# Optimization experiments

Hardware: AMD Instinct MI355X
Metric: run time of the kernel (lower is better)

Reference implementation:

```python
import jax, jax.numpy as jnp
import numpy as np

# Model dims (Mamba2-2.7B-like)
B_SZ = 1; SEQ = 2048; HID = 2048
INTER = 4096; N_STATE = 128; N_GROUPS = 1; NH = 64; HD = 64
K_CONV = 4; CHUNK = 256
GN = N_GROUPS * N_STATE            # 128
CONV_DIM = INTER + 2 * GN          # 4352
D_IN = 2 * INTER + 2 * GN + NH     # 8512
EPS = 1e-5


def setup_inputs() -> dict:
    key = jax.random.key(0)
    ks = jax.random.split(key, 8)
    return {
        "hidden_states": jax.random.normal(ks[0], (B_SZ, SEQ, HID), jnp.float32),
        "W_in": jax.random.normal(ks[1], (HID, D_IN), jnp.float32) * 0.02,
        "conv_w": jax.random.normal(ks[2], (CONV_DIM, K_CONV), jnp.float32) * 0.2,
        "conv_b": jax.random.normal(ks[3], (CONV_DIM,), jnp.float32) * 0.1,
        "dt_bias": jax.random.uniform(ks[4], (NH,), jnp.float32, -4.0, 0.0),
        "A": -jnp.exp(jax.random.uniform(ks[5], (NH,), jnp.float32, -1.0, 1.0)),
        "D": jnp.ones((NH,), jnp.float32),
        "norm_weight": jnp.ones((INTER,), jnp.float32),
        "W_out": jax.random.normal(ks[6], (INTER, HID), jnp.float32) * 0.02,
    }


def reference(hidden_states, W_in, conv_w, conv_b, dt_bias, A, D, norm_weight, W_out):
    b, S, _ = hidden_states.shape
    # in_proj and split: gate [inter], x/B/C [conv_dim], dt [num_heads]
    proj = hidden_states @ W_in
    gate, xBC, dt = jnp.split(proj, [INTER, INTER + CONV_DIM], axis=-1)
    dt = jax.nn.softplus(dt + dt_bias)  # [b,S,NH]

    # causal depthwise conv1d + SiLU (kernel K, left-padded)
    xp = jnp.pad(xBC, ((0, 0), (K_CONV - 1, 0), (0, 0)))
    conv = conv_b
    for k in range(K_CONV):  # tiny fixed loop over kernel taps
        conv = conv + conv_w[:, k] * xp[:, k:k + S, :]
    xBC = jax.nn.silu(conv)

    x, Bm, Cm = jnp.split(xBC, [INTER, INTER + GN], axis=-1)
    L = CHUNK; nc = S // L
    x_c = x.reshape(b, nc, L, NH, HD)
    rep = NH // N_GROUPS
    B_c = jnp.repeat(Bm.reshape(b, nc, L, N_GROUPS, N_STATE), rep, axis=3)  # bclhn
    C_c = jnp.repeat(Cm.reshape(b, nc, L, N_GROUPS, N_STATE), rep, axis=3)
    dt_c = dt.reshape(b, nc, L, NH)

    dA = dt_c * A                      # [b,c,l,h]  (A < 0)
    cA = jnp.cumsum(dA, axis=2)        # within-chunk cumulative log-decay
    cAt = jnp.transpose(cA, (0, 1, 3, 2))  # [b,c,h,l]

    # intra-chunk: causal decay matrix, (C B^T) masked, weighted by dt
    diff = cAt[..., :, None] - cAt[..., None, :]          # [b,c,h,l,s]
    tril = jnp.tril(jnp.ones((L, L), bool))
    Lmat = jnp.exp(jnp.where(tril, diff, -jnp.inf))
    CB = jnp.einsum('bclhn,bcshn->bchls', C_c, B_c)
    M = CB * Lmat * jnp.transpose(dt_c, (0, 1, 3, 2))[:, :, :, None, :]
    Y_intra = jnp.einsum('bchls,bcshp->bclhp', M, x_c)

    # per-chunk end state contributions
    decay_states = jnp.exp(cA[:, :, -1:, :] - cA)          # [b,c,l,h]
    states = jnp.einsum('bclh,bclhn,bclhp->bchpn', decay_states * dt_c, B_c, x_c)
    chunk_decay = jnp.exp(cA[:, :, -1, :])                 # [b,c,h]

    def step(carry, inp):
        d, st = inp
        new = carry * d[..., None, None] + st
        return new, carry  # emit state entering the chunk

    _, prev = jax.lax.scan(step, jnp.zeros((b, NH, HD, N_STATE), states.dtype),
                           (jnp.moveaxis(chunk_decay, 1, 0), jnp.moveaxis(states, 1, 0)))
    prev = jnp.moveaxis(prev, 0, 1)                        # [b,c,h,p,n]

    Y_inter = jnp.einsum('bclhn,bclh,bchpn->bclhp', C_c, jnp.exp(cA), prev)
    Y = Y_intra + Y_inter + x_c * D[:, None]               # skip D*x per head

    y = Y.reshape(b, S, INTER)
    # gated RMSNorm in fp32
    z = y.astype(jnp.float32) * jax.nn.silu(gate.astype(jnp.float32))
    var = jnp.mean(z * z, axis=-1, keepdims=True)
    z = z * jax.lax.rsqrt(var + EPS) * norm_weight
    return z @ W_out
```

## Files before the change

kernel.cpp:

```cpp
#include <hip/hip_runtime.h>

typedef __bf16 bf16_t;
typedef bf16_t bf16x8 __attribute__((ext_vector_type(8)));
typedef float f32x4 __attribute__((ext_vector_type(4)));
typedef unsigned short u16;
typedef u16 u16x8 __attribute__((ext_vector_type(8)));
typedef u16 u16x4 __attribute__((ext_vector_type(4)));

#define SEQ   2048
#define HID   2048
#define INTER 4096
#define NH    64
#define HD    64
#define CONVD 4352
#define DIN   8512
#define LDP   8576L
#define CHNK  256
#define NC    8

__device__ __forceinline__ u16 f2bf(float f) {
  union { float f; unsigned u; } a; a.f = f;
  return (u16)((a.u + 0x7fffu + ((a.u >> 16) & 1u)) >> 16);
}
__device__ __forceinline__ float bf2f(u16 u) {
  union { unsigned u; float f; } a; a.u = ((unsigned)u) << 16;
  return a.f;
}

__device__ __forceinline__ void gl2lds16(const void* g, void* l) {
  auto gp = reinterpret_cast<__attribute__((address_space(1))) void*>(
      (unsigned long long)g);
  auto lp = reinterpret_cast<__attribute__((address_space(3))) void*>(
      (unsigned)(unsigned long long)l);
  __builtin_amdgcn_global_load_lds(gp, lp, 16, 0, 0);
}

__global__ __launch_bounds__(256) void cvt_bf16(const float* __restrict__ s,
                                                u16* __restrict__ d, int n4) {
  int i = blockIdx.x * 256 + threadIdx.x;
  if (i < n4) {
    f32x4 v = ((const f32x4*)s)[i];
    u16x4 r;
#pragma unroll
    for (int k = 0; k < 4; ++k) r[k] = f2bf(v[k]);
    ((u16x4*)d)[i] = r;
  }
}

__global__ void transpose_bf16(const float* __restrict__ src, u16* __restrict__ dst,
                               int R, int Cc) {
  __shared__ float t[32][33];
  int n0 = blockIdx.x * 32, k0 = blockIdx.y * 32;
  int tx = threadIdx.x, ty = threadIdx.y;
  for (int i = ty; i < 32; i += 8) {
    int n = n0 + tx;
    t[i][tx] = (n < Cc) ? src[(long)(k0 + i) * Cc + n] : 0.f;
  }
  __syncthreads();
  for (int i = ty; i < 32; i += 8)
    dst[(long)(n0 + i) * R + k0 + tx] = f2bf(t[tx][i]);
}

__global__ __launch_bounds__(256, 2) void gemm_bt(const u16* __restrict__ A,
                                                  const u16* __restrict__ Bt,
                                                  float* __restrict__ C,
                                                  int N, int lda, int Klen,
                                                  long zstride) {
  __shared__ __align__(16) u16 As[128 * 64];
  __shared__ __align__(16) u16 Bs[128 * 64];
  const int kz = blockIdx.z;
  A  += (long)kz * Klen;
  Bt += (long)kz * Klen;
  C  += (long)kz * zstride;
  const int nb = gridDim.x * gridDim.y;
  const int id = blockIdx.x + gridDim.x * blockIdx.y;
  const int s = (id & 7) * (nb >> 3) + (id >> 3);
  const long bm = s & 15;
  const long bn = s >> 4;

  const int tid = threadIdx.x;
  const int lane = tid & 63;
  const int w = tid >> 6;
  const int wm = w >> 1, wn = w & 1;

  f32x4 acc[4][4];
#pragma unroll
  for (int i = 0; i < 4; ++i)
#pragma unroll
    for (int j = 0; j < 4; ++j) acc[i][j] = (f32x4){0.f, 0.f, 0.f, 0.f};

  const int srr = lane >> 3;
  const int sc8 = ((lane & 7) ^ srr) * 8;
  const u16* Agw = A + (bm * 128 + w * 8 + srr) * (long)lda + sc8;
  const u16* Bgw = Bt + (bn * 128 + w * 8 + srr) * (long)lda + sc8;
  u16* ldA = As + w * 512 + lane * 8;
  u16* ldB = Bs + w * 512 + lane * 8;
  const int fr = lane & 15, q = lane >> 4;
  const int fx = (fr & 7) << 3;

  for (int k0 = 0; k0 < Klen; k0 += 64) {
    __syncthreads();
#pragma unroll
    for (int t = 0; t < 4; ++t) {
      gl2lds16(Agw + k0 + (long)t * 32 * lda, ldA + t * 2048);
      gl2lds16(Bgw + k0 + (long)t * 32 * lda, ldB + t * 2048);
    }
    __builtin_amdgcn_s_waitcnt(0);
    __syncthreads();
#pragma unroll
    for (int ks = 0; ks < 2; ++ks) {
      bf16x8 af[4], bfv[4];
#pragma unroll
      for (int i = 0; i < 4; ++i)
        af[i] = *(const bf16x8*)(As + ((wm * 64 + i * 16 + fr) << 6) +
                                 ((((ks << 2) + q) << 3) ^ fx));
#pragma unroll
      for (int j = 0; j < 4; ++j)
        bfv[j] = *(const bf16x8*)(Bs + ((wn * 64 + j * 16 + fr) << 6) +
                                  ((((ks << 2) + q) << 3) ^ fx));
#pragma unroll
      for (int i = 0; i < 4; ++i)
#pragma unroll
        for (int j = 0; j < 4; ++j)
          acc[i][j] = __builtin_amdgcn_mfma_f32_16x16x32_bf16(af[i], bfv[j], acc[i][j], 0, 0, 0);
    }
  }
  const int cr = (lane >> 4) * 4;
  const int cc = lane & 15;
#pragma unroll
  for (int i = 0; i < 4; ++i)
#pragma unroll
    for (int j = 0; j < 4; ++j) {
      long r = bm * 128 + wm * 64 + i * 16 + cr;
      long cidx = bn * 128 + wn * 64 + j * 16 + cc;
      float* cp = C + r * (long)N + cidx;
#pragma unroll
      for (int t = 0; t < 4; ++t) cp[(long)t * N] = acc[i][j][t];
    }
}

#define MFMA16(ACC, AF, BF)                                                    \
  _Pragma("unroll") for (int i_ = 0; i_ < 4; ++i_)                             \
  _Pragma("unroll") for (int j_ = 0; j_ < 2; ++j_) {                           \
    ACC[i_][j_] = __builtin_amdgcn_mfma_f32_16x16x32_bf16(                     \
        AF[i_][0], BF[j_][0], ACC[i_][j_], 0, 0, 0);                           \
    ACC[i_][j_] = __builtin_amdgcn_mfma_f32_16x16x32_bf16(                     \
        AF[i_][1], BF[j_][1], ACC[i_][j_], 0, 0, 0);                           \
  }

#define LDAF(DST, SLOT)                                                        \
  _Pragma("unroll") for (int i_ = 0; i_ < 4; ++i_) {                           \
    const u16* p_ = Abuf[SLOT] + ((wm * 64 + i_ * 16 + fr) << 6);              \
    DST[i_][0] = *(const bf16x8*)(p_ + ke0);                                   \
    DST[i_][1] = *(const bf16x8*)(p_ + ke1);                                   \
  }

#define LDBF(DST, SLOT)                                                        \
  _Pragma("unroll") for (int j_ = 0; j_ < 2; ++j_) {                           \
    const u16* p_ = Bbuf[SLOT] + ((wn * 32 + j_ * 16 + fr) << 6);              \
    DST[j_][0] = *(const bf16x8*)(p_ + ke0);                                   \
    DST[j_][1] = *(const bf16x8*)(p_ + ke1);                                   \
  }

#define STAGE(G, HO, KO, SLOT, BUF)                                            \
  {                                                                            \
    const u16* g_ = (G) + (HO) + (KO);                                         \
    gl2lds16(g_ + off1, BUF[SLOT] + lo1);                                      \
    gl2lds16(g_ + off2, BUF[SLOT] + lo2);                                      \
  }

__global__ __launch_bounds__(512, 2) void gemm256(const u16* __restrict__ A,
                                                  const u16* __restrict__ Bt,
                                                  float* __restrict__ C,
                                                  int N, int lda, int Klen,
                                                  long zstride) {
  __shared__ __align__(16) u16 Abuf[4][128 * 64];
  __shared__ __align__(16) u16 Bbuf[4][128 * 64];

  const int kz = blockIdx.z;
  A  += (long)kz * Klen;
  Bt += (long)kz * Klen;
  C  += (long)kz * zstride;

  const int nb = gridDim.x * gridDim.y;
  const int id = blockIdx.x + gridDim.x * blockIdx.y;
  const int s = (id & 7) * (nb >> 3) + (id >> 3);
  const long bm = s & 7;
  const long bn = s >> 3;

  const int tid = threadIdx.x;
  const int lane = tid & 63;
  const int w = tid >> 6;
  const int wm = w >> 2;
  const int wn = w & 3;
  const int fr = lane & 15, q = lane >> 4;
  const int ke0 = (q ^ (fr & 7)) << 3;
  const int ke1 = ((4 + q) ^ (fr & 7)) << 3;

  const int sr1 = (w << 4) + (lane >> 3);
  const int sr2 = sr1 + 8;
  const int kcp = lane & 7;
  const long off1 = (long)sr1 * lda + ((kcp ^ (sr1 & 7)) << 3);
  const long off2 = (long)sr2 * lda + ((kcp ^ (sr2 & 7)) << 3);
  const int lo1 = (w << 10) + (lane << 3);
  const int lo2 = lo1 + 512;
  const long h128 = 128L * lda;

  const u16* gA = A + bm * 256 * lda;
  const u16* gB = Bt + bn * 256 * lda;

  f32x4 acc00[4][2], acc01[4][2], acc10[4][2], acc11[4][2];
#pragma unroll
  for (int i = 0; i < 4; ++i)
#pragma unroll
    for (int j = 0; j < 2; ++j) {
      acc00[i][j] = (f32x4){0.f, 0.f, 0.f, 0.f};
      acc01[i][j] = (f32x4){0.f, 0.f, 0.f, 0.f};
      acc10[i][j] = (f32x4){0.f, 0.f, 0.f, 0.f};
      acc11[i][j] = (f32x4){0.f, 0.f, 0.f, 0.f};
    }

  const int NT = Klen >> 6;

  STAGE(gA, 0L, 0L, 0, Abuf);
  STAGE(gB, 0L, 0L, 0, Bbuf);
  STAGE(gB, h128, 0L, 1, Bbuf);
  STAGE(gA, h128, 0L, 1, Abuf);
  STAGE(gA, 0L, 64L, 2, Abuf);
  STAGE(gB, 0L, 64L, 2, Bbuf);
  asm volatile("s_waitcnt vmcnt(6)" ::: "memory");
  __builtin_amdgcn_s_barrier();

  for (int T = 0; T < NT; ++T) {
    const int t2 = (T << 1) & 3;
    const int t2p1 = (t2 + 1) & 3;
    const int t2p3 = (t2 + 3) & 3;
    const long kT1 = (long)(T + 1) << 6;
    const long kT2 = (long)(T + 2) << 6;
    const bool g1 = (T + 1 < NT), g2 = (T + 2 < NT);
    bf16x8 a0[4][2], a1[4][2], b0[2][2], b1[2][2];

    LDAF(a0, t2);
    LDBF(b0, t2);
    if (g1) STAGE(gB, h128, kT1, t2p3, Bbuf);
    __builtin_amdgcn_s_barrier();
    __builtin_amdgcn_s_setprio(1);
    MFMA16(acc00, a0, b0);
    __builtin_amdgcn_s_setprio(0);
    __builtin_amdgcn_s_barrier();

    LDBF(b1, t2p1);
    if (g1) STAGE(gA, h128, kT1, t2p3, Abuf);
    __builtin_amdgcn_s_barrier();
    __builtin_amdgcn_s_setprio(1);
    MFMA16(acc01, a0, b1);
    __builtin_amdgcn_s_setprio(0);
    asm volatile("s_waitcnt vmcnt(6)" ::: "memory");
    __builtin_amdgcn_s_barrier();

    LDAF(a1, t2p1);
    if (g2) STAGE(gA, 0L, kT2, t2, Abuf);
    __builtin_amdgcn_s_barrier();
    __builtin_amdgcn_s_setprio(1);
    MFMA16(acc10, a1, b0);
    __builtin_amdgcn_s_setprio(0);
    __builtin_amdgcn_s_barrier();

    if (g2) STAGE(gB, 0L, kT2, t2, Bbuf);
    __builtin_amdgcn_s_barrier();
    __builtin_amdgcn_s_setprio(1);
    MFMA16(acc11, a1, b1);
    __builtin_amdgcn_s_setprio(0);
    if (T == NT - 2)
      asm volatile("s_waitcnt vmcnt(0)" ::: "memory");
    else
      asm volatile("s_waitcnt vmcnt(6)" ::: "memory");
    __builtin_amdgcn_s_barrier();
  }

  const int cr = (lane >> 4) << 2;
  const int cc = lane & 15;
  const long r0 = bm * 256 + wm * 64 + cr;
  const long c0 = bn * 256 + wn * 32 + cc;
#define CWRITE(ACC, QA, QB)                                                    \
  _Pragma("unroll") for (int i_ = 0; i_ < 4; ++i_)                             \
  _Pragma("unroll") for (int j_ = 0; j_ < 2; ++j_) {                           \
    long r_ = r0 + (QA)*128 + i_ * 16;                                         \
    long c_ = c0 + (QB)*128 + j_ * 16;                                         \
    if (c_ < N) {                                                              \
      float* cp_ = C + r_ * (long)N + c_;                                      \
      _Pragma("unroll") for (int t_ = 0; t_ < 4; ++t_)                         \
          cp_[(long)t_ * N] = ACC[i_][j_][t_];                                 \
    }                                                                          \
  }
  CWRITE(acc00, 0, 0)
  CWRITE(acc01, 0, 1)
  CWRITE(acc10, 1, 0)
  CWRITE(acc11, 1, 1)
#undef CWRITE
}

__global__ __launch_bounds__(256) void add4_kernel(const float* __restrict__ a,
                                                   float* __restrict__ o) {
  int i = blockIdx.x * 256 + threadIdx.x;
  f32x4 r = ((const f32x4*)a)[i];
  r += ((const f32x4*)(a + 4194304L))[i];
  r += ((const f32x4*)(a + 8388608L))[i];
  r += ((const f32x4*)(a + 12582912L))[i];
  ((f32x4*)o)[i] = r;
}

__global__ __launch_bounds__(256) void conv_silu_t(const float* __restrict__ proj,
                                                   const float* __restrict__ cw,
                                                   const float* __restrict__ cb,
                                                   u16* __restrict__ xbf,
                                                   u16* __restrict__ xT) {
  __shared__ float ld[35][33];
  __shared__ u16 tt[32][34];
  const int c0 = blockIdx.x * 32, t0 = blockIdx.y * 32;
  const int tx = threadIdx.x & 31, ty = threadIdx.x >> 5;
  for (int i = ty; i < 35; i += 8) {
    int t = t0 - 3 + i;
    ld[i][tx] = (t >= 0) ? proj[(long)t * LDP + INTER + c0 + tx] : 0.f;
  }
  const int c = c0 + tx;
  const float w0 = cw[c * 4 + 0], w1 = cw[c * 4 + 1], w2 = cw[c * 4 + 2],
              w3 = cw[c * 4 + 3], bias = cb[c];
  __syncthreads();
  for (int i = ty; i < 32; i += 8) {
    float a = bias + w0 * ld[i][tx] + w1 * ld[i + 1][tx] + w2 * ld[i + 2][tx] +
              w3 * ld[i + 3][tx];
    u16 v = f2bf(a / (1.f + __expf(-a)));
    xbf[(long)(t0 + i) * CONVD + c] = v;
    tt[i][tx] = v;
  }
  __syncthreads();
  if (c0 < 4224) {
    for (int i = ty; i < 32; i += 8)
      xT[(long)(c0 + i) * 2048 + t0 + tx] = tt[tx][i];
  }
}

__global__ __launch_bounds__(256) void dt_cumsum(const float* __restrict__ proj,
                                                 const float* __restrict__ dtb,
                                                 const float* __restrict__ A,
                                                 float* __restrict__ dt2,
                                                 float* __restrict__ cA2) {
  __shared__ float sc[256];
  int c = blockIdx.x, h = blockIdx.y, l = threadIdx.x;
  float v = proj[(long)(c * 256 + l) * LDP + 8448 + h] + dtb[h];
  float sp = (v > 20.f) ? v : log1pf(__expf(v));
  dt2[h * 2048 + c * 256 + l] = sp;
  sc[l] = sp * A[h];
  __syncthreads();
  for (int off = 1; off < 256; off <<= 1) {
    float t = (l >= off) ? sc[l - off] : 0.f;
    __syncthreads();
    sc[l] += t;
    __syncthreads();
  }
  cA2[h * 2048 + c * 256 + l] = sc[l];
}

__global__ __launch_bounds__(256, 2) void cb_gemm(const u16* __restrict__ xbf,
                                                  float* __restrict__ CB) {
  __shared__ __align__(16) u16 As[128 * 32];
  __shared__ __align__(16) u16 Bs[128 * 32];
  const int tid = threadIdx.x;
  const int lane = tid & 63;
  const int w = tid >> 6;
  const int wm = w >> 1, wn = w & 1;
  const int bm = blockIdx.y, bn = blockIdx.x, c = blockIdx.z;

  f32x4 acc[4][4];
#pragma unroll
  for (int i = 0; i < 4; ++i)
#pragma unroll
    for (int j = 0; j < 4; ++j) acc[i][j] = (f32x4){0.f, 0.f, 0.f, 0.f};

  const int sr = w * 32 + (lane >> 2);
  const int sc = ((lane & 3) ^ ((lane >> 2) & 3)) * 8;
  const u16* Ag = xbf + (long)(c * 256 + bm * 128) * CONVD + 4224;
  const u16* Bg = xbf + (long)(c * 256 + bn * 128) * CONVD + 4096;
  u16* lA0 = As + w * 1024 + lane * 8;
  u16* lA1 = As + w * 1024 + 512 + lane * 8;
  u16* lB0 = Bs + w * 1024 + lane * 8;
  u16* lB1 = Bs + w * 1024 + 512 + lane * 8;
  const int fr = lane & 15, q = lane >> 4;
  const int pc = ((q ^ (fr & 3)) << 3);

  for (int k0 = 0; k0 < 128; k0 += 32) {
    __syncthreads();
    const u16* a0 = Ag + (long)sr * CONVD + k0 + sc;
    const u16* b0 = Bg + (long)sr * CONVD + k0 + sc;
    gl2lds16(a0, lA0);
    gl2lds16(a0 + 16L * CONVD, lA1);
    gl2lds16(b0, lB0);
    gl2lds16(b0 + 16L * CONVD, lB1);
    __builtin_amdgcn_s_waitcnt(0);
    __syncthreads();
    bf16x8 af[4], bfv[4];
#pragma unroll
    for (int i = 0; i < 4; ++i)
      af[i] = *(const bf16x8*)(As + ((wm * 64 + i * 16 + fr) << 5) + pc);
#pragma unroll
    for (int j = 0; j < 4; ++j)
      bfv[j] = *(const bf16x8*)(Bs + ((wn * 64 + j * 16 + fr) << 5) + pc);
#pragma unroll
    for (int i = 0; i < 4; ++i)
#pragma unroll
      for (int j = 0; j < 4; ++j)
        acc[i][j] = __builtin_amdgcn_mfma_f32_16x16x32_bf16(af[i], bfv[j], acc[i][j], 0, 0, 0);
  }
  const int cr = (lane >> 4) * 4;
  const int cc = lane & 15;
  float* Cc = CB + (long)c * 65536;
#pragma unroll
  for (int i = 0; i < 4; ++i)
#pragma unroll
    for (int j = 0; j < 4; ++j) {
      int r = bm * 128 + wm * 64 + i * 16 + cr;
      int cidx = bn * 128 + wn * 64 + j * 16 + cc;
      float* cp = Cc + (long)r * 256 + cidx;
#pragma unroll
      for (int t = 0; t < 4; ++t) cp[t * 256] = acc[i][j][t];
    }
}

#define LDM 72
__global__ __launch_bounds__(256) void states_kernel(const u16* __restrict__ xT,
                                                     const float* __restrict__ dt2,
                                                     const float* __restrict__ cA2,
                                                     float* __restrict__ stT) {
  __shared__ __align__(16) u16 Ms[128 * LDM];
  __shared__ __align__(16) u16 Xs[64 * LDM];
  __shared__ float wl[256];
  const int c = blockIdx.x, h = blockIdx.y;
  const int tid = threadIdx.x;
  const int lane = tid & 63, w = tid >> 6;
  const int fr = lane & 15, q = lane >> 4;
  {
    float calast = cA2[h * 2048 + c * 256 + 255];
    float ca = cA2[h * 2048 + c * 256 + tid];
    wl[tid] = __expf(calast - ca) * dt2[h * 2048 + c * 256 + tid];
  }
  f32x4 acc[2][4];
#pragma unroll
  for (int i = 0; i < 2; ++i)
#pragma unroll
    for (int j = 0; j < 4; ++j) acc[i][j] = (f32x4){0.f, 0.f, 0.f, 0.f};

  const int lc8 = (tid & 7) * 8;
  const int rn = tid >> 3;
  __syncthreads();

  for (int kt = 0; kt < 4; ++kt) {
    __syncthreads();
#pragma unroll
    for (int r = 0; r < 4; ++r) {
      int n = rn + 32 * r;
      u16x8 raw = *(const u16x8*)(xT + (long)(4096 + n) * 2048 + c * 256 + kt * 64 + lc8);
      union { u16 u[8]; bf16x8 v; } pk;
#pragma unroll
      for (int u = 0; u < 8; ++u)
        pk.u[u] = f2bf(bf2f(raw[u]) * wl[kt * 64 + lc8 + u]);
      *(bf16x8*)(Ms + n * LDM + lc8) = pk.v;
    }
#pragma unroll
    for (int r = 0; r < 2; ++r) {
      int p = rn + 32 * r;
      *(bf16x8*)(Xs + p * LDM + lc8) =
          *(const bf16x8*)(xT + (long)(h * 64 + p) * 2048 + c * 256 + kt * 64 + lc8);
    }
    __syncthreads();
#pragma unroll
    for (int ks = 0; ks < 64; ks += 32) {
      bf16x8 af[2], xf[4];
#pragma unroll
      for (int i = 0; i < 2; ++i)
        af[i] = *(const bf16x8*)(Ms + (w * 32 + i * 16 + fr) * LDM + ks + q * 8);
#pragma unroll
      for (int j = 0; j < 4; ++j)
        xf[j] = *(const bf16x8*)(Xs + (j * 16 + fr) * LDM + ks + q * 8);
#pragma unroll
      for (int i = 0; i < 2; ++i)
#pragma unroll
        for (int j = 0; j < 4; ++j)
          acc[i][j] = __builtin_amdgcn_mfma_f32_16x16x32_bf16(af[i], xf[j], acc[i][j], 0, 0, 0);
    }
  }
  const int cr = (lane >> 4) * 4;
  const int cc = lane & 15;
  float* outp = stT + (long)(c * 64 + h) * 8192;
#pragma unroll
  for (int i = 0; i < 2; ++i)
#pragma unroll
    for (int j = 0; j < 4; ++j) {
      int n = w * 32 + i * 16 + cr;
      int p = j * 16 + cc;
#pragma unroll
      for (int t = 0; t < 4; ++t) outp[(n + t) * 64 + p] = acc[i][j][t];
    }
}

__global__ __launch_bounds__(256) void scan_kernel(const float* __restrict__ stT,
                                                   const float* __restrict__ cA2,
                                                   float* __restrict__ prevT) {
  int id = blockIdx.x * 256 + threadIdx.x;
  int h = id >> 13;
  float acc = 0.f;
#pragma unroll
  for (int c = 0; c < NC; ++c) {
    prevT[(long)c * 524288 + id] = acc;
    float cd = __expf(cA2[h * 2048 + c * 256 + 255]);
    acc = acc * cd + stT[(long)c * 524288 + id];
  }
}

__global__ __launch_bounds__(256) void ssm_y_kernel(const u16* __restrict__ xbf,
                                                    const u16* __restrict__ xT,
                                                    const float* __restrict__ dt2,
                                                    const float* __restrict__ cA2,
                                                    const float* __restrict__ CB,
                                                    const float* __restrict__ prevT,
                                                    const float* __restrict__ Dp,
                                                    u16* __restrict__ Y) {
  __shared__ __align__(16) u16 Ms[256 * LDM];
  __shared__ __align__(16) u16 Xt[64 * LDM];
  __shared__ float cas[256];
  __shared__ float dts[256];
  const int c = blockIdx.x, h = blockIdx.y;
  const int tid = threadIdx.x;
  const int lane = tid & 63;
  const int w = tid >> 6;
  const int fr = lane & 15, q = lane >> 4;

  cas[tid] = cA2[h * 2048 + c * 256 + tid];
  dts[tid] = dt2[h * 2048 + c * 256 + tid];

  f32x4 acc[4][4];
#pragma unroll
  for (int i = 0; i < 4; ++i)
#pragma unroll
    for (int j = 0; j < 4; ++j) acc[i][j] = (f32x4){0.f, 0.f, 0.f, 0.f};

  const int sg = (tid & 7) * 8;
  const int lb = tid >> 3;
  const int xp = tid & 63;
  const int xq = tid >> 6;

  __syncthreads();

  for (int kt = 0; kt < 6; ++kt) {
    __syncthreads();
    if (kt < 4) {
      const int s0 = kt * 64;
      f32x4 e0 = *(const f32x4*)&cas[s0 + sg];
      f32x4 e1 = *(const f32x4*)&cas[s0 + sg + 4];
      f32x4 d0 = *(const f32x4*)&dts[s0 + sg];
      f32x4 d1 = *(const f32x4*)&dts[s0 + sg + 4];
#pragma unroll
      for (int k = 0; k < 8; ++k) {
        const int l = lb + 32 * k;
        const float cal = cas[l];
        const float* cb = CB + (long)c * 65536 + (long)l * 256 + s0 + sg;
        f32x4 c0 = *(const f32x4*)cb;
        f32x4 c1 = *(const f32x4*)(cb + 4);
        union { u16 u[8]; bf16x8 v; } pk;
#pragma unroll
        for (int u = 0; u < 8; ++u) {
          int s = s0 + sg + u;
          float cv = (u < 4) ? c0[u] : c1[u - 4];
          float cs = (u < 4) ? e0[u] : e1[u - 4];
          float dv = (u < 4) ? d0[u] : d1[u - 4];
          float m = (s <= l) ? cv * __expf(cal - cs) * dv : 0.f;
          pk.u[u] = f2bf(m);
        }
        *(bf16x8*)(Ms + l * LDM + sg) = pk.v;
      }
#pragma unroll
      for (int r = 0; r < 2; ++r) {
        int p = (tid >> 3) + 32 * r;
        *(bf16x8*)(Xt + p * LDM + sg) =
            *(const bf16x8*)(xT + (long)(h * 64 + p) * 2048 + c * 256 + s0 + sg);
      }
    } else {
      const int n0 = (kt - 4) * 64;
#pragma unroll
      for (int k = 0; k < 8; ++k) {
        const int l = lb + 32 * k;
        const float ea = __expf(cas[l]);
        u16x8 raw = *(const u16x8*)(xbf + (long)(c * 256 + l) * CONVD + 4224 + n0 + sg);
        union { u16 u[8]; bf16x8 v; } pk;
#pragma unroll
        for (int u = 0; u < 8; ++u) pk.u[u] = f2bf(ea * bf2f(raw[u]));
        *(bf16x8*)(Ms + l * LDM + sg) = pk.v;
      }
      const float* pT = prevT + (long)(c * 64 + h) * 8192;
#pragma unroll
      for (int half = 0; half < 2; ++half) {
        const int nb2 = xq * 16 + half * 8;
        union { u16 u[8]; bf16x8 v; } pk;
#pragma unroll
        for (int u = 0; u < 8; ++u) pk.u[u] = f2bf(pT[(n0 + nb2 + u) * 64 + xp]);
        *(bf16x8*)(Xt + xp * LDM + nb2) = pk.v;
      }
    }
    __syncthreads();
#pragma unroll
    for (int ks = 0; ks < 64; ks += 32) {
      bf16x8 af[4], bfv[4];
#pragma unroll
      for (int i = 0; i < 4; ++i)
        af[i] = *(const bf16x8*)(Ms + (w * 64 + i * 16 + fr) * LDM + ks + q * 8);
#pragma unroll
      for (int j = 0; j < 4; ++j)
        bfv[j] = *(const bf16x8*)(Xt + (j * 16 + fr) * LDM + ks + q * 8);
#pragma unroll
      for (int i = 0; i < 4; ++i)
#pragma unroll
        for (int j = 0; j < 4; ++j)
          acc[i][j] = __builtin_amdgcn_mfma_f32_16x16x32_bf16(af[i], bfv[j], acc[i][j], 0, 0, 0);
    }
  }

  const int cr = (lane >> 4) * 4;
  const int cc = lane & 15;
  const float dh = Dp[h];
#pragma unroll
  for (int i = 0; i < 4; ++i)
#pragma unroll
    for (int j = 0; j < 4; ++j) {
      const int p = j * 16 + cc;
#pragma unroll
      for (int t = 0; t < 4; ++t) {
        const int row = w * 64 + i * 16 + cr + t;
        const float xv = bf2f(xbf[(long)(c * 256 + row) * CONVD + h * 64 + p]);
        Y[(long)(c * 256 + row) * 4096 + h * 64 + p] = f2bf(acc[i][j][t] + dh * xv);
      }
    }
}

__global__ __launch_bounds__(256) void rmsnorm_kernel(const u16* __restrict__ Y,
                                                      const float* __restrict__ proj,
                                                      const float* __restrict__ nw,
                                                      u16* __restrict__ zbf) {
  __shared__ float red[256];
  int t = blockIdx.x, tid = threadIdx.x;
  const u16* y = Y + (long)t * 4096;
  const float* g = proj + (long)t * LDP;
  float zv[16];
  float s = 0.f;
#pragma unroll
  for (int k = 0; k < 16; ++k) {
    int i = tid + k * 256;
    float gv = g[i];
    float z = bf2f(y[i]) * (gv / (1.f + __expf(-gv)));
    zv[k] = z;
    s += z * z;
  }
  red[tid] = s;
  __syncthreads();
  if (tid < 128) red[tid] += red[tid + 128];
  __syncthreads();
  if (tid < 64) {
    float v = red[tid] + red[tid + 64];
    v += __shfl_down(v, 32);
    v += __shfl_down(v, 16);
    v += __shfl_down(v, 8);
    v += __shfl_down(v, 4);
    v += __shfl_down(v, 2);
    v += __shfl_down(v, 1);
    if (tid == 0) red[0] = v;
  }
  __syncthreads();
  float scale = rsqrtf(red[0] * (1.f / 4096.f) + 1e-5f);
#pragma unroll
  for (int k = 0; k < 16; ++k) {
    int i = tid + k * 256;
    zbf[(long)t * 4096 + i] = f2bf(zv[k] * scale * nw[i]);
  }
}

extern "C" void kernel_launch(void* const* d_in, const int* in_sizes, int n_in,
                              void* d_out, int out_size, void* d_ws, size_t ws_size,
                              hipStream_t stream) {
  const float* hidden = (const float*)d_in[0];
  const float* Win    = (const float*)d_in[1];
  const float* convw  = (const float*)d_in[2];
  const float* convb  = (const float*)d_in[3];
  const float* dtb    = (const float*)d_in[4];
  const float* Ap     = (const float*)d_in[5];
  const float* Dp     = (const float*)d_in[6];
  const float* nw     = (const float*)d_in[7];
  const float* Wout   = (const float*)d_in[8];
  float* out = (float*)d_out;
  char* ws = (char*)d_ws;

  u16*   hb    = (u16*)(ws + 0);
  u16*   WinT  = (u16*)(ws + 8388608L);
  float* proj  = (float*)(ws + 43515904L);
  u16*   WoutT = (u16*)(ws + 113770496L);
  u16*   xbf   = (u16*)(ws + 130547712L);
  u16*   xT    = (u16*)(ws + 148373504L);
  float* dt2   = (float*)(ws + 165675008L);
  float* cA2   = (float*)(ws + 166199296L);
  float* CBv   = (float*)(ws + 166723584L);
  float* stT   = (float*)(ws + 168820736L);
  float* prevT = (float*)(ws + 185597952L);
  u16*   zbf   = (u16*)(ws + 202375168L);
  u16*   Y     = (u16*)(ws + 0);
  float* Cp    = (float*)(ws + 43515904L);

  cvt_bf16<<<4096, 256, 0, stream>>>(hidden, hb, 1048576);
  transpose_bf16<<<dim3(268, 64), dim3(32, 8), 0, stream>>>(Win, WinT, 2048, 8512);
  transpose_bf16<<<dim3(64, 128), dim3(32, 8), 0, stream>>>(Wout, WoutT, 4096, 2048);
  gemm256<<<dim3(32, 8, 1), 512, 0, stream>>>(hb, WinT, proj, 8576, 2048, 2048, 0L);
  gemm_bt<<<dim3(3, 16, 1), 256, 0, stream>>>(hb, WinT + 8192L * 2048, proj + 8192,
                                              8576, 2048, 2048, 0L);
  conv_silu_t<<<dim3(136, 64), 256, 0, stream>>>(proj, convw, convb, xbf, xT);
  dt_cumsum<<<dim3(8, 64), 256, 0, stream>>>(proj, dtb, Ap, dt2, cA2);
  cb_gemm<<<dim3(2, 2, 8), 256, 0, stream>>>(xbf, CBv);
  states_kernel<<<dim3(8, 64), 256, 0, stream>>>(xT, dt2, cA2, stT);
  scan_kernel<<<2048, 256, 0, stream>>>(stT, cA2, prevT);
  ssm_y_kernel<<<dim3(8, 64), 256, 0, stream>>>(xbf, xT, dt2, cA2, CBv, prevT, Dp, Y);
  rmsnorm_kernel<<<2048, 256, 0, stream>>>(Y, proj, nw, zbf);
  gemm256<<<dim3(8, 8, 4), 512, 0, stream>>>(zbf, WoutT, Cp, 2048, 4096, 1024, 4194304L);
  add4_kernel<<<4096, 256, 0, stream>>>(Cp, out);
}
```

Measured before the change: 418.5 us.

## Split-K the in_proj tail strip GEMM and hand-schedule LDS reads in gemm256

The leftover 320-column strip of the input projection was computed by a small 48-block gemm_bt launch. It is now split four ways along K into a scratch buffer, and a new strip_add kernel sums the partials into proj, which raises parallelism for that launch. Separately, the gemm256 LDS fragment loads are replaced with inline ds_read_b128 asm, with explicit lgkmcnt waits and sched_barrier fences before each MFMA phase to pin down instruction ordering. This costs an extra kernel launch and partial-sum traffic, and the fences may serialize LDS latency against the MFMAs.

Measured after the change: 406.1 us. -3.0%, faster.

```diff
diff --git a/kernel.cpp b/kernel.cpp
--- a/kernel.cpp
+++ b/kernel.cpp
@@ -33,6 +33,12 @@
   auto lp = reinterpret_cast<__attribute__((address_space(3))) void*>(
       (unsigned)(unsigned long long)l);
   __builtin_amdgcn_global_load_lds(gp, lp, 16, 0, 0);
+}
+
+__device__ __forceinline__ bf16x8 ds128(unsigned addr) {
+  bf16x8 r;
+  asm volatile("ds_read_b128 %0, %1" : "=v"(r) : "v"(addr));
+  return r;
 }
 
 __global__ __launch_bounds__(256) void cvt_bf16(const float* __restrict__ s,
@@ -149,17 +155,23 @@
   }
 
 #define LDAF(DST, SLOT)                                                        \
-  _Pragma("unroll") for (int i_ = 0; i_ < 4; ++i_) {                           \
-    const u16* p_ = Abuf[SLOT] + ((wm * 64 + i_ * 16 + fr) << 6);              \
-    DST[i_][0] = *(const bf16x8*)(p_ + ke0);                                   \
-    DST[i_][1] = *(const bf16x8*)(p_ + ke1);                                   \
+  {                                                                            \
+    unsigned ab_ = (unsigned)(unsigned long long)(&Abuf[SLOT][0]);             \
+    _Pragma("unroll") for (int i_ = 0; i_ < 4; ++i_) {                         \
+      unsigned ro_ = ab_ + (((wm * 64 + i_ * 16 + fr) << 6) << 1);             \
+      DST[i_][0] = ds128(ro_ + (ke0 << 1));                                    \
+      DST[i_][1] = ds128(ro_ + (ke1 << 1));                                    \
+    }                                                                          \
   }
 
 #define LDBF(DST, SLOT)                                                        \
-  _Pragma("unroll") for (int j_ = 0; j_ < 2; ++j_) {                           \
-    const u16* p_ = Bbuf[SLOT] + ((wn * 32 + j_ * 16 + fr) << 6);              \
-    DST[j_][0] = *(const bf16x8*)(p_ + ke0);                                   \
-    DST[j_][1] = *(const bf16x8*)(p_ + ke1);                                   \
+  {                                                                            \
+    unsigned bb_ = (unsigned)(unsigned long long)(&Bbuf[SLOT][0]);             \
+    _Pragma("unroll") for (int j_ = 0; j_ < 2; ++j_) {                         \
+      unsigned ro_ = bb_ + (((wn * 32 + j_ * 16 + fr) << 6) << 1);             \
+      DST[j_][0] = ds128(ro_ + (ke0 << 1));                                    \
+      DST[j_][1] = ds128(ro_ + (ke1 << 1));                                    \
+    }                                                                          \
   }
 
 #define STAGE(G, HO, KO, SLOT, BUF)                                            \
@@ -168,6 +180,10 @@
     gl2lds16(g_ + off1, BUF[SLOT] + lo1);                                      \
     gl2lds16(g_ + off2, BUF[SLOT] + lo2);                                      \
   }
+
+#define PH_FENCE()                                                             \
+  asm volatile("s_waitcnt lgkmcnt(0)" ::: "memory");                           \
+  __builtin_amdgcn_sched_barrier(0);
 
 __global__ __launch_bounds__(512, 2) void gemm256(const u16* __restrict__ A,
                                                   const u16* __restrict__ Bt,
@@ -243,7 +259,9 @@
     LDAF(a0, t2);
     LDBF(b0, t2);
     if (g1) STAGE(gB, h128, kT1, t2p3, Bbuf);
+    asm volatile("s_waitcnt lgkmcnt(8)" ::: "memory");
     __builtin_amdgcn_s_barrier();
+    PH_FENCE();
     __builtin_amdgcn_s_setprio(1);
     MFMA16(acc00, a0, b0);
     __builtin_amdgcn_s_setprio(0);
@@ -252,6 +270,7 @@
     LDBF(b1, t2p1);
     if (g1) STAGE(gA, h128, kT1, t2p3, Abuf);
     __builtin_amdgcn_s_barrier();
+    PH_FENCE();
     __builtin_amdgcn_s_setprio(1);
     MFMA16(acc01, a0, b1);
     __builtin_amdgcn_s_setprio(0);
@@ -261,6 +280,7 @@
     LDAF(a1, t2p1);
     if (g2) STAGE(gA, 0L, kT2, t2, Abuf);
     __builtin_amdgcn_s_barrier();
+    PH_FENCE();
     __builtin_amdgcn_s_setprio(1);
     MFMA16(acc10, a1, b0);
     __builtin_amdgcn_s_setprio(0);
@@ -268,6 +288,7 @@
 
     if (g2) STAGE(gB, 0L, kT2, t2, Bbuf);
     __builtin_amdgcn_s_barrier();
+    PH_FENCE();
     __builtin_amdgcn_s_setprio(1);
     MFMA16(acc11, a1, b1);
     __builtin_amdgcn_s_setprio(0);
@@ -308,6 +329,17 @@
   r += ((const f32x4*)(a + 8388608L))[i];
   r += ((const f32x4*)(a + 12582912L))[i];
   ((f32x4*)o)[i] = r;
+}
+
+__global__ __launch_bounds__(256) void strip_add(const float* __restrict__ a,
+                                                 float* __restrict__ proj) {
+  int g = blockIdx.x * 256 + threadIdx.x;
+  int r = g / 96, c4 = g - r * 96;
+  f32x4 v = ((const f32x4*)a)[g];
+  v += ((const f32x4*)(a + 786432L))[g];
+  v += ((const f32x4*)(a + 1572864L))[g];
+  v += ((const f32x4*)(a + 2359296L))[g];
+  ((f32x4*)(proj + (long)r * LDP + 8192))[c4] = v;
 }
 
 __global__ __launch_bounds__(256) void conv_silu_t(const float* __restrict__ proj,
@@ -711,13 +743,15 @@
   u16*   zbf   = (u16*)(ws + 202375168L);
   u16*   Y     = (u16*)(ws + 0);
   float* Cp    = (float*)(ws + 43515904L);
+  float* Cs    = (float*)(ws + 168820736L);
 
   cvt_bf16<<<4096, 256, 0, stream>>>(hidden, hb, 1048576);
   transpose_bf16<<<dim3(268, 64), dim3(32, 8), 0, stream>>>(Win, WinT, 2048, 8512);
   transpose_bf16<<<dim3(64, 128), dim3(32, 8), 0, stream>>>(Wout, WoutT, 4096, 2048);
   gemm256<<<dim3(32, 8, 1), 512, 0, stream>>>(hb, WinT, proj, 8576, 2048, 2048, 0L);
-  gemm_bt<<<dim3(3, 16, 1), 256, 0, stream>>>(hb, WinT + 8192L * 2048, proj + 8192,
-                                              8576, 2048, 2048, 0L);
+  gemm_bt<<<dim3(3, 16, 4), 256, 0, stream>>>(hb, WinT + 8192L * 2048, Cs,
+                                              384, 2048, 512, 786432L);
+  strip_add<<<768, 256, 0, stream>>>(Cs, proj);
   conv_silu_t<<<dim3(136, 64), 256, 0, stream>>>(proj, convw, convb, xbf, xT);
   dt_cumsum<<<dim3(8, 64), 256, 0, stream>>>(proj, dtb, Ap, dt2, cA2);
   cb_gemm<<<dim3(2, 2, 8), 256, 0, stream>>>(xbf, CBv);
```
